# Optimization experiments

Measured on AMD Instinct MI355X. Metric: run time of the kernel, lower is better.

Reference implementation:

```python
import jax, jax.numpy as jnp
import numpy as np

N_USERS = 50000
N_ITEMS = 100000
N_NODES = N_USERS + N_ITEMS
N_EDGES = 2400000
D = 64
N_LAYERS = 3


def setup_inputs() -> dict:
    key = jax.random.key(0)
    ks = jax.random.split(key, 9)
    edge_src = jax.random.randint(ks[0], (N_EDGES,), 0, N_NODES, dtype=jnp.int32)
    edge_dst = jax.random.randint(ks[1], (N_EDGES,), 0, N_NODES, dtype=jnp.int32)
    edge_vals = jax.random.uniform(ks[2], (N_EDGES,), dtype=jnp.float32)
    user_emb = jax.random.normal(ks[3], (N_USERS, D), dtype=jnp.float32) * 0.1
    item_emb = jax.random.normal(ks[4], (N_ITEMS, D), dtype=jnp.float32) * 0.1
    Wgc = jax.random.normal(ks[5], (N_LAYERS, D, D), dtype=jnp.float32) * (1.0 / np.sqrt(D))
    bgc = jax.random.normal(ks[6], (N_LAYERS, D), dtype=jnp.float32) * 0.01
    Wbi = jax.random.normal(ks[7], (N_LAYERS, D, D), dtype=jnp.float32) * (1.0 / np.sqrt(D))
    bbi = jax.random.normal(ks[8], (N_LAYERS, D), dtype=jnp.float32) * 0.01
    return {"edge_src": edge_src, "edge_dst": edge_dst, "edge_vals": edge_vals,
            "user_emb": user_emb, "item_emb": item_emb,
            "Wgc": Wgc, "bgc": bgc, "Wbi": Wbi, "bbi": bbi}


def _spmm(edge_src, edge_dst, edge_vals, x, n_nodes):
    # adj @ x with adj in COO: out[d] = sum_e vals[e] * x[src[e]] for dst[e]==d
    msgs = edge_vals[:, None] * x[edge_src]          # [E, D]
    return jax.ops.segment_sum(msgs, edge_dst, num_segments=n_nodes)


def _l2norm(x, eps=1e-12):
    n = jnp.sqrt(jnp.sum(x * x, axis=1, keepdims=True))
    return x / jnp.maximum(n, eps)


def reference(edge_src, edge_dst, edge_vals, user_emb, item_emb, Wgc, bgc, Wbi, bbi):
    n_users = user_emb.shape[0]
    n_nodes = n_users + item_emb.shape[0]
    ego = jnp.concatenate([user_emb, item_emb], axis=0)  # [N, D]
    all_embs = [ego]
    for i in range(Wgc.shape[0]):
        side = _spmm(edge_src, edge_dst, edge_vals, ego, n_nodes)       # adj @ ego
        sum_e = jax.nn.leaky_relu(side @ Wgc[i].T + bgc[i])             # GC branch
        bi_e = jax.nn.leaky_relu((ego * side) @ Wbi[i].T + bbi[i])      # Bi branch
        ego = sum_e + bi_e                                              # dropout p=0 -> identity
        all_embs.append(_l2norm(ego))
    all_embs = jnp.concatenate(all_embs, axis=1)  # [N, D*(L+1)]
    return all_embs[:n_users], all_embs[n_users:]
```

## Files before the change

kernel.cpp:

```cpp
#include <hip/hip_runtime.h>

#define NU 50000
#define NI 100000
#define NN 150000
#define NE 2400000
#define DD 64
#define NL 3
#define CHUNK 1024
#define NB ((NN + CHUNK - 1) / CHUNK)

__global__ void init_kernel(const float* __restrict__ uemb, const float* __restrict__ iemb,
                            float* __restrict__ ego, float* __restrict__ out) {
    int i = blockIdx.x * blockDim.x + threadIdx.x;
    if (i >= NN * DD) return;
    int n = i >> 6, d = i & 63;
    float v = (n < NU) ? uemb[i] : iemb[i - NU * DD];
    ego[i] = v;
    out[n * (DD * (NL + 1)) + d] = v;
}

__global__ void hist_kernel(const int* __restrict__ dst, int* __restrict__ counts) {
    int e = blockIdx.x * blockDim.x + threadIdx.x;
    if (e < NE) atomicAdd(&counts[dst[e]], 1);
}

__global__ void scanA_kernel(const int* __restrict__ counts, int* __restrict__ bsum) {
    __shared__ int sh[256];
    int t = threadIdx.x, b = blockIdx.x;
    int base = b * CHUNK + t * 4;
    int s = 0;
#pragma unroll
    for (int i = 0; i < 4; ++i) { int idx = base + i; if (idx < NN) s += counts[idx]; }
    sh[t] = s; __syncthreads();
    for (int off = 128; off > 0; off >>= 1) {
        if (t < off) sh[t] += sh[t + off];
        __syncthreads();
    }
    if (t == 0) bsum[b] = sh[0];
}

__global__ void scanB_kernel(int* __restrict__ bsum, int* __restrict__ offs) {
    __shared__ int sh[256];
    int t = threadIdx.x;
    int v = (t < NB) ? bsum[t] : 0;
    sh[t] = v; __syncthreads();
    for (int off = 1; off < 256; off <<= 1) {
        int add = (t >= off) ? sh[t - off] : 0;
        __syncthreads();
        sh[t] += add;
        __syncthreads();
    }
    if (t < NB) bsum[t] = sh[t] - v;
    if (t == NB - 1) offs[NN] = sh[t];
}

__global__ void scanC_kernel(const int* __restrict__ counts, const int* __restrict__ bsum,
                             int* __restrict__ offs) {
    __shared__ int sh[256];
    int t = threadIdx.x, b = blockIdx.x;
    int base = b * CHUNK + t * 4;
    int c[4]; int tsum = 0;
#pragma unroll
    for (int i = 0; i < 4; ++i) { int idx = base + i; c[i] = (idx < NN) ? counts[idx] : 0; tsum += c[i]; }
    sh[t] = tsum; __syncthreads();
    for (int off = 1; off < 256; off <<= 1) {
        int add = (t >= off) ? sh[t - off] : 0;
        __syncthreads();
        sh[t] += add;
        __syncthreads();
    }
    int excl = sh[t] - tsum + bsum[b];
#pragma unroll
    for (int i = 0; i < 4; ++i) {
        int idx = base + i;
        if (idx < NN) offs[idx] = excl;
        excl += c[i];
    }
}

__global__ void fill_kernel(const int* __restrict__ src, const int* __restrict__ dst,
                            const float* __restrict__ vals, const int* __restrict__ offs,
                            int* __restrict__ cursor, int2* __restrict__ pair) {
    int e = blockIdx.x * blockDim.x + threadIdx.x;
    if (e >= NE) return;
    int d = dst[e];
    int pos = offs[d] + atomicAdd(&cursor[d], 1);
    pair[pos] = make_int2(src[e], __float_as_int(vals[e]));
}

__global__ __launch_bounds__(256) void spmm_kernel(
        const int* __restrict__ offs, const int2* __restrict__ pair,
        const float* __restrict__ ego, float* __restrict__ side) {
    int gid = blockIdx.x * blockDim.x + threadIdx.x;
    int node = gid >> 6;
    if (node >= NN) return;
    int lane = threadIdx.x & 63;
    int sub = lane >> 4;
    int dq  = lane & 15;
    int beg = offs[node], end = offs[node + 1];
    float4 acc = make_float4(0.f, 0.f, 0.f, 0.f);
    int i = beg;
    for (; i + 4 <= end; i += 4) {
        int2 p = pair[i + sub];
        float w = __int_as_float(p.y);
        float4 v = ((const float4*)(ego + (size_t)p.x * DD))[dq];
        acc.x = fmaf(w, v.x, acc.x);
        acc.y = fmaf(w, v.y, acc.y);
        acc.z = fmaf(w, v.z, acc.z);
        acc.w = fmaf(w, v.w, acc.w);
    }
    if (i < end) {
        int r = end - i;
        if (sub < r) {
            int2 p = pair[i + sub];
            float w = __int_as_float(p.y);
            float4 v = ((const float4*)(ego + (size_t)p.x * DD))[dq];
            acc.x = fmaf(w, v.x, acc.x);
            acc.y = fmaf(w, v.y, acc.y);
            acc.z = fmaf(w, v.z, acc.z);
            acc.w = fmaf(w, v.w, acc.w);
        }
    }
    acc.x += __shfl_xor(acc.x, 16); acc.y += __shfl_xor(acc.y, 16);
    acc.z += __shfl_xor(acc.z, 16); acc.w += __shfl_xor(acc.w, 16);
    acc.x += __shfl_xor(acc.x, 32); acc.y += __shfl_xor(acc.y, 32);
    acc.z += __shfl_xor(acc.z, 32); acc.w += __shfl_xor(acc.w, 32);
    if (sub == 0) ((float4*)(side + (size_t)node * DD))[dq] = acc;
}

typedef float v2f __attribute__((ext_vector_type(2)));
#define UPD_TPB 256
#define UPD_GRID 1024
#define NPAIR (NN / 2)

__global__ __launch_bounds__(UPD_TPB, 3) void update_kernel(
        const float* __restrict__ side, float* __restrict__ ego,
        const float* __restrict__ Wg, const float* __restrict__ bg,
        const float* __restrict__ Wb, const float* __restrict__ bb,
        float* __restrict__ out, int layer) {
    __shared__ v2f sm[UPD_TPB / 64][2][DD];
    int tid = threadIdx.x;
    int lane = tid & 63;
    int wid = tid >> 6;

    v2f w[DD];
    {
        const float4* g4 = (const float4*)(Wg + lane * DD);
        const float4* b4 = (const float4*)(Wb + lane * DD);
#pragma unroll
        for (int k4 = 0; k4 < 16; ++k4) {
            float4 a = g4[k4], b = b4[k4];
            w[4 * k4 + 0] = (v2f){a.x, b.x};
            w[4 * k4 + 1] = (v2f){a.y, b.y};
            w[4 * k4 + 2] = (v2f){a.z, b.z};
            w[4 * k4 + 3] = (v2f){a.w, b.w};
        }
    }
    v2f bias = {bg[lane], bb[lane]};

    const int nwaves = UPD_GRID * (UPD_TPB / 64);
    int g = blockIdx.x * (UPD_TPB / 64) + wid;
    if (g >= NPAIR) return;

    float s0 = side[(size_t)(2 * g) * DD + lane];
    float s1 = side[(size_t)(2 * g + 1) * DD + lane];
    float e0 = ego[(size_t)(2 * g) * DD + lane];
    float e1 = ego[(size_t)(2 * g + 1) * DD + lane];

    while (true) {
        sm[wid][0][lane] = (v2f){s0, s0 * e0};
        sm[wid][1][lane] = (v2f){s1, s1 * e1};

        int gn = g + nwaves;
        bool more = gn < NPAIR;
        int gl = more ? gn : g;
        s0 = side[(size_t)(2 * gl) * DD + lane];
        s1 = side[(size_t)(2 * gl + 1) * DD + lane];
        e0 = ego[(size_t)(2 * gl) * DD + lane];
        e1 = ego[(size_t)(2 * gl + 1) * DD + lane];

        v2f acc0 = bias, acc1 = bias;
#pragma unroll
        for (int k = 0; k < DD; ++k) {
            v2f a = sm[wid][0][k];
            v2f b = sm[wid][1][k];
            acc0 = __builtin_elementwise_fma(a, w[k], acc0);
            acc1 = __builtin_elementwise_fma(b, w[k], acc1);
        }

        float ag0 = acc0.x, ab0 = acc0.y, ag1 = acc1.x, ab1 = acc1.y;
        ag0 = (ag0 > 0.f) ? ag0 : 0.01f * ag0;
        ab0 = (ab0 > 0.f) ? ab0 : 0.01f * ab0;
        ag1 = (ag1 > 0.f) ? ag1 : 0.01f * ag1;
        ab1 = (ab1 > 0.f) ? ab1 : 0.01f * ab1;
        float v0 = ag0 + ab0, v1 = ag1 + ab1;
        float sq0 = v0 * v0, sq1 = v1 * v1;
#pragma unroll
        for (int off = 1; off < 64; off <<= 1) {
            sq0 += __shfl_xor(sq0, off);
            sq1 += __shfl_xor(sq1, off);
        }
        float r0 = 1.f / fmaxf(sqrtf(sq0), 1e-12f);
        float r1 = 1.f / fmaxf(sqrtf(sq1), 1e-12f);
        int n0 = 2 * g;
        ego[(size_t)n0 * DD + lane] = v0;
        ego[(size_t)(n0 + 1) * DD + lane] = v1;
        out[(size_t)n0 * (DD * (NL + 1)) + (layer + 1) * DD + lane] = v0 * r0;
        out[(size_t)(n0 + 1) * (DD * (NL + 1)) + (layer + 1) * DD + lane] = v1 * r1;

        if (!more) break;
        g = gn;
    }
}

extern "C" void kernel_launch(void* const* d_in, const int* in_sizes, int n_in,
                              void* d_out, int out_size, void* d_ws, size_t ws_size,
                              hipStream_t stream) {
    const int*   edge_src  = (const int*)d_in[0];
    const int*   edge_dst  = (const int*)d_in[1];
    const float* edge_vals = (const float*)d_in[2];
    const float* uemb      = (const float*)d_in[3];
    const float* iemb      = (const float*)d_in[4];
    const float* Wgc       = (const float*)d_in[5];
    const float* bgc       = (const float*)d_in[6];
    const float* Wbi       = (const float*)d_in[7];
    const float* bbi       = (const float*)d_in[8];
    float* out = (float*)d_out;

    char* p = (char*)d_ws;
    auto alloc = [&](size_t bytes) { char* r = p; p += (bytes + 255) & ~(size_t)255; return r; };
    int*   counts = (int*)alloc((size_t)NN * 4);
    int*   offs   = (int*)alloc((size_t)(NN + 1) * 4);
    int*   bsum   = (int*)alloc((size_t)NB * 4);
    int2*  pair   = (int2*)alloc((size_t)NE * 8);
    float* ego    = (float*)alloc((size_t)NN * DD * 4);
    float* side   = (float*)alloc((size_t)NN * DD * 4);

    hipMemsetAsync(counts, 0, (size_t)NN * 4, stream);
    init_kernel<<<(NN * DD + 255) / 256, 256, 0, stream>>>(uemb, iemb, ego, out);
    hist_kernel<<<(NE + 255) / 256, 256, 0, stream>>>(edge_dst, counts);
    scanA_kernel<<<NB, 256, 0, stream>>>(counts, bsum);
    scanB_kernel<<<1, 256, 0, stream>>>(bsum, offs);
    scanC_kernel<<<NB, 256, 0, stream>>>(counts, bsum, offs);
    hipMemsetAsync(counts, 0, (size_t)NN * 4, stream);
    fill_kernel<<<(NE + 255) / 256, 256, 0, stream>>>(edge_src, edge_dst, edge_vals, offs, counts, pair);

    for (int l = 0; l < NL; ++l) {
        spmm_kernel<<<(NN * 64 + 255) / 256, 256, 0, stream>>>(offs, pair, ego, side);
        update_kernel<<<UPD_GRID, UPD_TPB, 0, stream>>>(
            side, ego, Wgc + l * DD * DD, bgc + l * DD, Wbi + l * DD * DD, bbi + l * DD,
            out, l);
    }
}
```

Measured before the change: 944.6 us.

## Record edge ranks in histogram, prefetch CSR pairs in SpMM, pack update LDS

```diff
diff --git a/kernel.cpp b/kernel.cpp
--- a/kernel.cpp
+++ b/kernel.cpp
@@ -19,9 +19,13 @@
     out[n * (DD * (NL + 1)) + d] = v;
 }
 
-__global__ void hist_kernel(const int* __restrict__ dst, int* __restrict__ counts) {
+__global__ void hist_kernel(const int* __restrict__ dst, int* __restrict__ counts,
+                            unsigned short* __restrict__ rank) {
     int e = blockIdx.x * blockDim.x + threadIdx.x;
-    if (e < NE) atomicAdd(&counts[dst[e]], 1);
+    if (e < NE) {
+        int r = atomicAdd(&counts[dst[e]], 1);
+        rank[e] = (unsigned short)r;
+    }
 }
 
 __global__ void scanA_kernel(const int* __restrict__ counts, int* __restrict__ bsum) {
@@ -80,11 +84,11 @@
 
 __global__ void fill_kernel(const int* __restrict__ src, const int* __restrict__ dst,
                             const float* __restrict__ vals, const int* __restrict__ offs,
-                            int* __restrict__ cursor, int2* __restrict__ pair) {
+                            const unsigned short* __restrict__ rank, int2* __restrict__ pair) {
     int e = blockIdx.x * blockDim.x + threadIdx.x;
     if (e >= NE) return;
     int d = dst[e];
-    int pos = offs[d] + atomicAdd(&cursor[d], 1);
+    int pos = offs[d] + (int)rank[e];
     pair[pos] = make_int2(src[e], __float_as_int(vals[e]));
 }
 
@@ -99,26 +103,23 @@
     int dq  = lane & 15;
     int beg = offs[node], end = offs[node + 1];
     float4 acc = make_float4(0.f, 0.f, 0.f, 0.f);
-    int i = beg;
-    for (; i + 4 <= end; i += 4) {
-        int2 p = pair[i + sub];
-        float w = __int_as_float(p.y);
-        float4 v = ((const float4*)(ego + (size_t)p.x * DD))[dq];
-        acc.x = fmaf(w, v.x, acc.x);
-        acc.y = fmaf(w, v.y, acc.y);
-        acc.z = fmaf(w, v.z, acc.z);
-        acc.w = fmaf(w, v.w, acc.w);
-    }
-    if (i < end) {
-        int r = end - i;
-        if (sub < r) {
-            int2 p = pair[i + sub];
-            float w = __int_as_float(p.y);
+    if (beg < end) {
+        int idx0 = beg + sub;
+        int2 p = pair[idx0 < end ? idx0 : end - 1];
+        for (int i = beg; i < end; i += 4) {
+            int2 pn = p;
+            int ni = i + 4;
+            if (ni < end) {
+                int nidx = ni + sub;
+                pn = pair[nidx < end ? nidx : end - 1];
+            }
+            float w = (i + sub < end) ? __int_as_float(p.y) : 0.f;
             float4 v = ((const float4*)(ego + (size_t)p.x * DD))[dq];
             acc.x = fmaf(w, v.x, acc.x);
             acc.y = fmaf(w, v.y, acc.y);
             acc.z = fmaf(w, v.z, acc.z);
             acc.w = fmaf(w, v.w, acc.w);
+            p = pn;
         }
     }
     acc.x += __shfl_xor(acc.x, 16); acc.y += __shfl_xor(acc.y, 16);
@@ -138,7 +139,7 @@
         const float* __restrict__ Wg, const float* __restrict__ bg,
         const float* __restrict__ Wb, const float* __restrict__ bb,
         float* __restrict__ out, int layer) {
-    __shared__ v2f sm[UPD_TPB / 64][2][DD];
+    __shared__ float4 sm[UPD_TPB / 64][DD];
     int tid = threadIdx.x;
     int lane = tid & 63;
     int wid = tid >> 6;
@@ -168,8 +169,7 @@
     float e1 = ego[(size_t)(2 * g + 1) * DD + lane];
 
     while (true) {
-        sm[wid][0][lane] = (v2f){s0, s0 * e0};
-        sm[wid][1][lane] = (v2f){s1, s1 * e1};
+        sm[wid][lane] = make_float4(s0, s0 * e0, s1, s1 * e1);
 
         int gn = g + nwaves;
         bool more = gn < NPAIR;
@@ -180,12 +180,11 @@
         e1 = ego[(size_t)(2 * gl + 1) * DD + lane];
 
         v2f acc0 = bias, acc1 = bias;
-#pragma unroll
+#pragma unroll 8
         for (int k = 0; k < DD; ++k) {
-            v2f a = sm[wid][0][k];
-            v2f b = sm[wid][1][k];
-            acc0 = __builtin_elementwise_fma(a, w[k], acc0);
-            acc1 = __builtin_elementwise_fma(b, w[k], acc1);
+            float4 q = sm[wid][k];
+            acc0 = __builtin_elementwise_fma((v2f){q.x, q.y}, w[k], acc0);
+            acc1 = __builtin_elementwise_fma((v2f){q.z, q.w}, w[k], acc1);
         }
 
         float ag0 = acc0.x, ab0 = acc0.y, ag1 = acc1.x, ab1 = acc1.y;
@@ -235,15 +234,15 @@
     int2*  pair   = (int2*)alloc((size_t)NE * 8);
     float* ego    = (float*)alloc((size_t)NN * DD * 4);
     float* side   = (float*)alloc((size_t)NN * DD * 4);
+    unsigned short* rank = (unsigned short*)alloc((size_t)NE * 2);
 
     hipMemsetAsync(counts, 0, (size_t)NN * 4, stream);
     init_kernel<<<(NN * DD + 255) / 256, 256, 0, stream>>>(uemb, iemb, ego, out);
-    hist_kernel<<<(NE + 255) / 256, 256, 0, stream>>>(edge_dst, counts);
+    hist_kernel<<<(NE + 255) / 256, 256, 0, stream>>>(edge_dst, counts, rank);
     scanA_kernel<<<NB, 256, 0, stream>>>(counts, bsum);
     scanB_kernel<<<1, 256, 0, stream>>>(bsum, offs);
     scanC_kernel<<<NB, 256, 0, stream>>>(counts, bsum, offs);
-    hipMemsetAsync(counts, 0, (size_t)NN * 4, stream);
-    fill_kernel<<<(NE + 255) / 256, 256, 0, stream>>>(edge_src, edge_dst, edge_vals, offs, counts, pair);
+    fill_kernel<<<(NE + 255) / 256, 256, 0, stream>>>(edge_src, edge_dst, edge_vals, offs, rank, pair);
 
     for (int l = 0; l < NL; ++l) {
         spmm_kernel<<<(NN * 64 + 255) / 256, 256, 0, stream>>>(offs, pair, ego, side);
```

New measurement: 1.754 ms. 85.7% more time.
